# Optimization experiments

Measured on AMD Instinct MI355X. Metric: run time of the kernel, lower is better.

The kernel has to match this reference:

```python
import jax, jax.numpy as jnp
import numpy as np


def setup_inputs() -> dict:
    key = jax.random.key(0)
    k1, k2, k3, k4, k5 = jax.random.split(key, 5)
    B, S, D, H, E = 4, 4096, 1024, 1024, 8  # H = per-expert hidden (fuel_dim)
    std = 0.02
    return {
        "hidden_states": jax.random.normal(k1, (B, S, D), dtype=jnp.float32),
        "gate_w": jax.random.normal(k2, (D, E), dtype=jnp.float32) * std,
        "gw": jax.random.normal(k3, (E, D, H), dtype=jnp.float32) * std,
        "pw": jax.random.normal(k4, (E, D, H), dtype=jnp.float32) * std,
        "ow": jax.random.normal(k5, (E, H, D), dtype=jnp.float32) * std,
        "top_k": 2,
    }


def reference(hidden_states, gate_w, gw, pw, ow, top_k):
    B, S, D = hidden_states.shape
    E = gate_w.shape[1]
    x = hidden_states.reshape(-1, D)  # [T, D]
    T = x.shape[0]

    # Router
    router_logits = x @ gate_w  # [T, E]
    routing_probs = jax.nn.softmax(router_logits.astype(jnp.float32), axis=-1)
    top_w, top_i = jax.lax.top_k(routing_probs, top_k)  # [T, k]
    top_w = top_w / jnp.sum(top_w, axis=-1, keepdims=True)
    top_w = top_w.astype(x.dtype)

    # Dense combine weights: zero for unselected experts -> same math as
    # the torch gather/expert/scatter loop.
    combine = jnp.zeros((T, E), dtype=x.dtype).at[
        jnp.arange(T)[:, None], top_i
    ].set(top_w)  # [T, E]

    # SwiGLU experts, batched over the expert dim.
    g = jnp.einsum('td,edh->eth', x, gw)          # [E, T, H]
    p = jnp.einsum('td,edh->eth', x, pw)          # [E, T, H]
    h = g * jax.nn.silu(p)                        # [E, T, H]
    y = jnp.einsum('eth,ehd->etd', h, ow)         # [E, T, D]
    final = jnp.einsum('etd,te->td', y, combine)  # [T, D]
    final = final.reshape(B, S, D)

    # Load-balancing loss (recomputes softmax/topk as the torch fn does)
    expert_mask = jax.nn.one_hot(top_i, E, dtype=jnp.float32)  # [T, k, E]
    tokens_per_expert = jnp.mean(expert_mask, axis=0)          # [k, E]
    router_prob_per_expert = jnp.mean(routing_probs, axis=0)   # [E]
    bl_loss = jnp.sum(tokens_per_expert * router_prob_per_expert[None, :]) * E

    return final, router_logits, bl_loss
```

## Files before the change

### kernel.cpp

```cpp
#include <hip/hip_runtime.h>
#include <hip/hip_bf16.h>
#include <cstdint>

#define T_TOK 16384
#define DDIM  1024

typedef __attribute__((ext_vector_type(8))) short bf16x8;
typedef __attribute__((ext_vector_type(4))) float f32x4;

__device__ __forceinline__ unsigned short f2bf(float f) {
  unsigned u = __builtin_bit_cast(unsigned, f);
  return (unsigned short)((u + 0x7fffu + ((u >> 16) & 1u)) >> 16);
}
__device__ __forceinline__ unsigned pk2(float a, float b) {
  return (unsigned)f2bf(a) | ((unsigned)f2bf(b) << 16);
}
__device__ __forceinline__ void gload16(const void* g, void* l) {
  typedef __attribute__((address_space(1))) const unsigned int gu32;
  typedef __attribute__((address_space(3))) unsigned int lu32;
  __builtin_amdgcn_global_load_lds((gu32*)g, (lu32*)l, 16, 0, 0);
}

#define SBAR()                        \
  __builtin_amdgcn_sched_barrier(0);  \
  __builtin_amdgcn_s_barrier();       \
  __builtin_amdgcn_sched_barrier(0)
#define WAIT_VM8()                                        \
  asm volatile("s_waitcnt vmcnt(8)" ::: "memory");        \
  __builtin_amdgcn_sched_barrier(0)
#define WAIT_VM0()                                        \
  asm volatile("s_waitcnt vmcnt(0)" ::: "memory");        \
  __builtin_amdgcn_sched_barrier(0)
#define WAIT_LGKM0()                                      \
  asm volatile("s_waitcnt lgkmcnt(0)" ::: "memory");      \
  __builtin_amdgcn_sched_barrier(0)

__global__ __launch_bounds__(256) void convert_k(
    const float* __restrict__ gw, const float* __restrict__ pw,
    const float* __restrict__ ow, char* __restrict__ wg,
    char* __restrict__ wp, char* __restrict__ wo) {
  __shared__ float t[64][65];
  const int z = blockIdx.z;
  const int arr = z >> 3, e = z & 7;
  const float* src = (arr == 0 ? gw : arr == 1 ? pw : ow) + ((long)e << 20);
  char* dst = (arr == 0 ? wg : arr == 1 ? wp : wo) + ((long)e << 21);
  const int r0 = blockIdx.x * 64, c0 = blockIdx.y * 64;
  const int row = threadIdx.x >> 2, q = threadIdx.x & 3;
  const float4* sp = (const float4*)(src + (long)(r0 + row) * 1024 + c0 + q * 16);
  float4 v0 = sp[0], v1 = sp[1], v2 = sp[2], v3 = sp[3];
  float* tr = &t[row][q * 16];
  tr[0]=v0.x; tr[1]=v0.y; tr[2]=v0.z; tr[3]=v0.w;
  tr[4]=v1.x; tr[5]=v1.y; tr[6]=v1.z; tr[7]=v1.w;
  tr[8]=v2.x; tr[9]=v2.y; tr[10]=v2.z; tr[11]=v2.w;
  tr[12]=v3.x; tr[13]=v3.y; tr[14]=v3.z; tr[15]=v3.w;
  __syncthreads();
  const int cl = row, rq = q;
  uint4 o0, o1;
  o0.x = pk2(t[rq*16+ 0][cl], t[rq*16+ 1][cl]);
  o0.y = pk2(t[rq*16+ 2][cl], t[rq*16+ 3][cl]);
  o0.z = pk2(t[rq*16+ 4][cl], t[rq*16+ 5][cl]);
  o0.w = pk2(t[rq*16+ 6][cl], t[rq*16+ 7][cl]);
  o1.x = pk2(t[rq*16+ 8][cl], t[rq*16+ 9][cl]);
  o1.y = pk2(t[rq*16+10][cl], t[rq*16+11][cl]);
  o1.z = pk2(t[rq*16+12][cl], t[rq*16+13][cl]);
  o1.w = pk2(t[rq*16+14][cl], t[rq*16+15][cl]);
  char* dp = dst + (long)(c0 + cl) * 2048 + (long)(r0 + rq * 16) * 2;
  *(uint4*)dp = o0;
  *(uint4*)(dp + 16) = o1;
}

__global__ __launch_bounds__(256) void router_k(
    const float* __restrict__ x, const float* __restrict__ gatew,
    float* __restrict__ logitsOut, float4* __restrict__ route,
    float* __restrict__ accum, unsigned short* __restrict__ xbo) {
  __shared__ float accB[16];
  const int tid = threadIdx.x;
  if (tid < 16) accB[tid] = 0.f;
  __syncthreads();
  const int lane = tid & 63;
  const int gwave = blockIdx.x * 4 + (tid >> 6);

  for (int g = gwave; g < 4096; g += 1024) {
    const int t0 = g * 4;
    float s[4][8];
#pragma unroll
    for (int tt = 0; tt < 4; ++tt)
#pragma unroll
      for (int e = 0; e < 8; ++e) s[tt][e] = 0.f;

    for (int i = 0; i < 16; ++i) {
      int d = lane + i * 64;
      float4 w0 = *(const float4*)(gatew + d * 8);
      float4 w1 = *(const float4*)(gatew + d * 8 + 4);
#pragma unroll
      for (int tt = 0; tt < 4; ++tt) {
        float xv = x[(long)(t0 + tt) * DDIM + d];
        if (xbo) xbo[(long)(t0 + tt) * DDIM + d] = f2bf(xv);
        s[tt][0] += xv * w0.x; s[tt][1] += xv * w0.y;
        s[tt][2] += xv * w0.z; s[tt][3] += xv * w0.w;
        s[tt][4] += xv * w1.x; s[tt][5] += xv * w1.y;
        s[tt][6] += xv * w1.z; s[tt][7] += xv * w1.w;
      }
    }
#pragma unroll
    for (int m = 1; m < 64; m <<= 1)
#pragma unroll
      for (int tt = 0; tt < 4; ++tt)
#pragma unroll
        for (int e = 0; e < 8; ++e) s[tt][e] += __shfl_xor(s[tt][e], m);

    float psum[8];
#pragma unroll
    for (int e = 0; e < 8; ++e) psum[e] = 0.f;
    int i1a[4], i2a[4];
    float w1a[4], w2a[4];
#pragma unroll
    for (int tt = 0; tt < 4; ++tt) {
      float mx = s[tt][0];
#pragma unroll
      for (int e = 1; e < 8; ++e) mx = fmaxf(mx, s[tt][e]);
      float pe[8], Z = 0.f;
#pragma unroll
      for (int e = 0; e < 8; ++e) { pe[e] = __expf(s[tt][e] - mx); Z += pe[e]; }
      float inv = 1.f / Z;
#pragma unroll
      for (int e = 0; e < 8; ++e) { pe[e] *= inv; psum[e] += pe[e]; }
      int i1 = 0; float p1 = pe[0];
#pragma unroll
      for (int e = 1; e < 8; ++e) if (pe[e] > p1) { p1 = pe[e]; i1 = e; }
      int i2 = -1; float p2 = -1.f;
#pragma unroll
      for (int e = 0; e < 8; ++e)
        if (e != i1 && pe[e] > p2) { p2 = pe[e]; i2 = e; }
      float wsum = p1 + p2;
      i1a[tt] = i1; i2a[tt] = i2;
      w1a[tt] = p1 / wsum; w2a[tt] = p2 / wsum;
    }
    if (lane < 32) {
      int tt = lane >> 3, e = lane & 7;
      logitsOut[(t0 + tt) * 8 + e] = s[tt][e];
    }
    if (lane < 32 && (lane & 7) == 0) {
      int tt = lane >> 3;
      float4 rr;
      rr.x = w1a[tt]; rr.y = w2a[tt];
      rr.z = __int_as_float(i1a[tt]); rr.w = __int_as_float(i2a[tt]);
      route[t0 + tt] = rr;
    }
    if (lane < 8) {
      float c = 0.f;
#pragma unroll
      for (int tt = 0; tt < 4; ++tt)
        c += (float)(i1a[tt] == lane) + (float)(i2a[tt] == lane);
      atomicAdd(&accB[lane], psum[lane]);
      atomicAdd(&accB[8 + lane], c);
    }
  }
  __syncthreads();
  if (tid < 16) atomicAdd(&accum[tid], accB[tid]);
}

__global__ void offsets_k(const float* __restrict__ accum,
                          int* __restrict__ offs, int* __restrict__ cursor,
                          int* __restrict__ cumT) {
  if (threadIdx.x == 0) {
    int c = 0;
#pragma unroll
    for (int e = 0; e < 8; ++e) {
      offs[e] = c; cursor[e] = c;
      c += (int)(accum[8 + e] + 0.5f);
    }
    offs[8] = c;
    int t = 0;
#pragma unroll
    for (int e = 0; e < 8; ++e) {
      cumT[e] = t;
      t += (offs[e + 1] - offs[e] + 255) >> 8;
    }
    cumT[8] = t;
  }
}

__global__ __launch_bounds__(256) void scatter_k(
    const float4* __restrict__ route, int* __restrict__ cursor,
    int* __restrict__ list, float* __restrict__ wsl) {
  int t = blockIdx.x * 256 + threadIdx.x;
  float4 rr = route[t];
  int i1 = __float_as_int(rr.z), i2 = __float_as_int(rr.w);
  int s1 = atomicAdd(&cursor[i1], 1);
  list[s1] = t; wsl[s1] = rr.x;
  int s2 = atomicAdd(&cursor[i2], 1);
  list[s2] = t; wsl[s2] = rr.y;
}

template <int XB>
__global__ __launch_bounds__(512, 2) void pass1_k(
    const float* __restrict__ x, const unsigned short* __restrict__ xb,
    const char* __restrict__ wg, const char* __restrict__ wp,
    const int* __restrict__ list, const float* __restrict__ wsl,
    const int* __restrict__ offs, const int* __restrict__ cumT,
    char* __restrict__ hw) {
  __shared__ __align__(16) char Al[2][32768];
  __shared__ __align__(16) char Bgl[2][16384];
  __shared__ __align__(16) char Bpl[2][16384];
  const int b = blockIdx.x;
  if (b >= cumT[8]) return;
  int e = 0;
#pragma unroll
  for (int i = 1; i < 8; ++i) e += (b >= cumT[i]);
  const int tile = b - cumT[e];
  const int start = offs[e] + tile * 256;
  const int valid = min(256, offs[e + 1] - start);
  const int chunk = blockIdx.y;
  const int tid = threadIdx.x, lane = tid & 63, wid = tid >> 6;

  const int l8 = lane >> 3, seg = lane & 7;
  const unsigned inrow = ((unsigned)(seg * 16)) ^ (((unsigned)l8) << 4);

  const char* asrc[4];
  unsigned adst[4];
#pragma unroll
  for (int i = 0; i < 4; ++i) {
    int row = wid * 32 + i * 8 + l8;
    int tok = list[start + min(row, valid - 1)];
    asrc[i] = (const char*)xb + ((long)tok << 11) + inrow;
    adst[i] = (unsigned)(wid * 4096 + i * 1024);
  }
  const long wbase = ((long)e << 21) + ((long)(chunk * 128) << 11);
  const char* gsrc[2];
  const char* psrc[2];
  unsigned bdst[2];
#pragma unroll
  for (int i = 0; i < 2; ++i) {
    int h = wid * 16 + i * 8 + l8;
    gsrc[i] = wg + wbase + ((long)h << 11) + inrow;
    psrc[i] = wp + wbase + ((long)h << 11) + inrow;
    bdst[i] = (unsigned)(wid * 2048 + i * 1024);
  }

  f32x4 aG[8][2], aP[8][2];
#pragma unroll
  for (int f = 0; f < 8; ++f)
#pragma unroll
    for (int j = 0; j < 2; ++j) {
      aG[f][j] = (f32x4){0.f, 0.f, 0.f, 0.f};
      aP[f][j] = (f32x4){0.f, 0.f, 0.f, 0.f};
    }

  const int col = lane & 15, kg = lane >> 4;
  const int mb = (wid >> 2) * 128, nb = (wid & 3) * 32;

#define P1_STAGE(kb, buf)                                     \
  {                                                           \
    long ko = (long)(kb) << 7;                                \
    gload16(asrc[0] + ko, &Al[buf][adst[0]]);                 \
    gload16(asrc[1] + ko, &Al[buf][adst[1]]);                 \
    gload16(asrc[2] + ko, &Al[buf][adst[2]]);                 \
    gload16(asrc[3] + ko, &Al[buf][adst[3]]);                 \
    gload16(gsrc[0] + ko, &Bgl[buf][bdst[0]]);                \
    gload16(gsrc[1] + ko, &Bgl[buf][bdst[1]]);                \
    gload16(psrc[0] + ko, &Bpl[buf][bdst[0]]);                \
    gload16(psrc[1] + ko, &Bpl[buf][bdst[1]]);                \
  }

  if (XB) {
    P1_STAGE(0, 0);
#pragma unroll 1
    for (int kb = 0; kb < 16; ++kb) {
      const int cur = kb & 1;
      if (kb < 15) {
        P1_STAGE(kb + 1, cur ^ 1);
        WAIT_VM8();
      } else {
        WAIT_VM0();
      }
      SBAR();
#pragma unroll
      for (int ks = 0; ks < 2; ++ks) {
        bf16x8 bg[2], bp[2], af[4];
#pragma unroll
        for (int j = 0; j < 2; ++j) {
          int n = nb + j * 16 + col;
          unsigned off = (unsigned)(n * 128 + ks * 64 + kg * 16) ^
                         (((unsigned)n & 7u) << 4);
          bg[j] = *(const bf16x8*)(&Bgl[cur][0] + off);
          bp[j] = *(const bf16x8*)(&Bpl[cur][0] + off);
        }
#pragma unroll
        for (int f = 0; f < 4; ++f) {
          int r = mb + f * 16 + col;
          af[f] = *(const bf16x8*)(
              &Al[cur][0] + ((unsigned)(r * 128 + ks * 64 + kg * 16) ^
                             (((unsigned)r & 7u) << 4)));
        }
        WAIT_LGKM0();
        __builtin_amdgcn_s_setprio(1);
#pragma unroll
        for (int f = 0; f < 4; ++f)
#pragma unroll
          for (int j = 0; j < 2; ++j) {
            aG[f][j] = __builtin_amdgcn_mfma_f32_16x16x32_bf16(
                af[f], bg[j], aG[f][j], 0, 0, 0);
            aP[f][j] = __builtin_amdgcn_mfma_f32_16x16x32_bf16(
                af[f], bp[j], aP[f][j], 0, 0, 0);
          }
        __builtin_amdgcn_s_setprio(0);
        SBAR();
#pragma unroll
        for (int f = 0; f < 4; ++f) {
          int r = mb + (f + 4) * 16 + col;
          af[f] = *(const bf16x8*)(
              &Al[cur][0] + ((unsigned)(r * 128 + ks * 64 + kg * 16) ^
                             (((unsigned)r & 7u) << 4)));
        }
        WAIT_LGKM0();
        __builtin_amdgcn_s_setprio(1);
#pragma unroll
        for (int f = 0; f < 4; ++f)
#pragma unroll
          for (int j = 0; j < 2; ++j) {
            aG[f + 4][j] = __builtin_amdgcn_mfma_f32_16x16x32_bf16(
                af[f], bg[j], aG[f + 4][j], 0, 0, 0);
            aP[f + 4][j] = __builtin_amdgcn_mfma_f32_16x16x32_bf16(
                af[f], bp[j], aP[f + 4][j], 0, 0, 0);
          }
        __builtin_amdgcn_s_setprio(0);
        SBAR();
      }
    }
  } else {
    const int sr2 = tid >> 1, q2 = tid & 1;
    const int tokS = list[start + min(sr2, valid - 1)];
    const float* axp = x + (long)tokS * DDIM + q2 * 32;
    const unsigned swzS = ((unsigned)(sr2 & 7)) << 4;
    const unsigned sbS = (unsigned)(sr2 * 128 + q2 * 64);
#pragma unroll 1
    for (int kb = 0; kb < 16; ++kb) {
      __syncthreads();
      {
        const float4* ap = (const float4*)(axp + kb * 64);
#pragma unroll
        for (int m = 0; m < 4; ++m) {
          float4 v0 = ap[m * 2], v1 = ap[m * 2 + 1];
          uint4 w;
          w.x = pk2(v0.x, v0.y); w.y = pk2(v0.z, v0.w);
          w.z = pk2(v1.x, v1.y); w.w = pk2(v1.z, v1.w);
          *(uint4*)(&Al[0][0] + ((sbS + m * 16) ^ swzS)) = w;
        }
        long ko = (long)kb << 7;
        gload16(gsrc[0] + ko, &Bgl[0][bdst[0]]);
        gload16(gsrc[1] + ko, &Bgl[0][bdst[1]]);
        gload16(psrc[0] + ko, &Bpl[0][bdst[0]]);
        gload16(psrc[1] + ko, &Bpl[0][bdst[1]]);
      }
      __syncthreads();
#pragma unroll
      for (int ks = 0; ks < 2; ++ks) {
        bf16x8 bg[2], bp[2];
#pragma unroll
        for (int j = 0; j < 2; ++j) {
          int n = nb + j * 16 + col;
          unsigned off = (unsigned)(n * 128 + ks * 64 + kg * 16) ^
                         (((unsigned)n & 7u) << 4);
          bg[j] = *(const bf16x8*)(&Bgl[0][0] + off);
          bp[j] = *(const bf16x8*)(&Bpl[0][0] + off);
        }
#pragma unroll
        for (int f = 0; f < 8; ++f) {
          int r = mb + f * 16 + col;
          bf16x8 a = *(const bf16x8*)(
              &Al[0][0] + ((unsigned)(r * 128 + ks * 64 + kg * 16) ^
                           (((unsigned)r & 7u) << 4)));
#pragma unroll
          for (int j = 0; j < 2; ++j) {
            aG[f][j] = __builtin_amdgcn_mfma_f32_16x16x32_bf16(
                a, bg[j], aG[f][j], 0, 0, 0);
            aP[f][j] = __builtin_amdgcn_mfma_f32_16x16x32_bf16(
                a, bp[j], aP[f][j], 0, 0, 0);
          }
        }
      }
    }
  }

  const int rg = lane >> 4;
#pragma unroll
  for (int f = 0; f < 8; ++f) {
#pragma unroll
    for (int r = 0; r < 4; ++r) {
      int ml = mb + f * 16 + rg * 4 + r;
      if (ml < valid) {
        int slot = start + ml;
        float wv = wsl[slot];
#pragma unroll
        for (int j = 0; j < 2; ++j) {
          float g = aG[f][j][r], p = aP[f][j][r];
          float h = g * (p / (1.f + __expf(-p))) * wv;
          int hc = chunk * 128 + nb + j * 16 + col;
          *(unsigned short*)(hw + (((long)slot << 11) + (hc << 1))) = f2bf(h);
        }
      }
    }
  }
}

__global__ __launch_bounds__(512, 2) void pass2_k(
    const char* __restrict__ hw, const char* __restrict__ wo,
    const int* __restrict__ list, const int* __restrict__ offs,
    const int* __restrict__ cumT, float* __restrict__ out) {
  __shared__ __align__(16) char Al[2][32768];
  __shared__ __align__(16) char Bl[2][32768];
  const int b = blockIdx.x;
  if (b >= cumT[8]) return;
  int e = 0;
#pragma unroll
  for (int i = 1; i < 8; ++i) e += (b >= cumT[i]);
  const int tile = b - cumT[e];
  const int start = offs[e] + tile * 256;
  const int valid = min(256, offs[e + 1] - start);
  const int chunk = blockIdx.y;
  const int tid = threadIdx.x, lane = tid & 63, wid = tid >> 6;

  const int l8 = lane >> 3, seg = lane & 7;
  const unsigned inrow = ((unsigned)(seg * 16)) ^ (((unsigned)l8) << 4);

  const char* asrc[4];
  const char* bsrc[4];
  unsigned dst4[4];
#pragma unroll
  for (int i = 0; i < 4; ++i) {
    int row = wid * 32 + i * 8 + l8;
    asrc[i] = hw + ((long)(start + min(row, valid - 1)) << 11) + inrow;
    bsrc[i] = wo + ((long)e << 21) + ((long)(chunk * 256 + row) << 11) + inrow;
    dst4[i] = (unsigned)(wid * 4096 + i * 1024);
  }

  f32x4 acc[8][4];
#pragma unroll
  for (int f = 0; f < 8; ++f)
#pragma unroll
    for (int j = 0; j < 4; ++j) acc[f][j] = (f32x4){0.f, 0.f, 0.f, 0.f};

  const int col = lane & 15, kg = lane >> 4;
  const int mb = (wid >> 2) * 128, nb = (wid & 3) * 64;

#define P2_STAGE(kb, buf)                                     \
  {                                                           \
    long ko = (long)(kb) << 7;                                \
    gload16(asrc[0] + ko, &Al[buf][dst4[0]]);                 \
    gload16(asrc[1] + ko, &Al[buf][dst4[1]]);                 \
    gload16(asrc[2] + ko, &Al[buf][dst4[2]]);                 \
    gload16(asrc[3] + ko, &Al[buf][dst4[3]]);                 \
    gload16(bsrc[0] + ko, &Bl[buf][dst4[0]]);                 \
    gload16(bsrc[1] + ko, &Bl[buf][dst4[1]]);                 \
    gload16(bsrc[2] + ko, &Bl[buf][dst4[2]]);                 \
    gload16(bsrc[3] + ko, &Bl[buf][dst4[3]]);                 \
  }

  P2_STAGE(0, 0);
#pragma unroll 1
  for (int kb = 0; kb < 16; ++kb) {
    const int cur = kb & 1;
    if (kb < 15) {
      P2_STAGE(kb + 1, cur ^ 1);
      WAIT_VM8();
    } else {
      WAIT_VM0();
    }
    SBAR();
#pragma unroll
    for (int ks = 0; ks < 2; ++ks) {
      bf16x8 bf4[4], af[4];
#pragma unroll
      for (int j = 0; j < 4; ++j) {
        int n = nb + j * 16 + col;
        bf4[j] = *(const bf16x8*)(
            &Bl[cur][0] + ((unsigned)(n * 128 + ks * 64 + kg * 16) ^
                           (((unsigned)n & 7u) << 4)));
      }
#pragma unroll
      for (int f = 0; f < 4; ++f) {
        int r = mb + f * 16 + col;
        af[f] = *(const bf16x8*)(
            &Al[cur][0] + ((unsigned)(r * 128 + ks * 64 + kg * 16) ^
                           (((unsigned)r & 7u) << 4)));
      }
      WAIT_LGKM0();
      __builtin_amdgcn_s_setprio(1);
#pragma unroll
      for (int f = 0; f < 4; ++f)
#pragma unroll
        for (int j = 0; j < 4; ++j)
          acc[f][j] = __builtin_amdgcn_mfma_f32_16x16x32_bf16(
              af[f], bf4[j], acc[f][j], 0, 0, 0);
      __builtin_amdgcn_s_setprio(0);
      SBAR();
#pragma unroll
      for (int f = 0; f < 4; ++f) {
        int r = mb + (f + 4) * 16 + col;
        af[f] = *(const bf16x8*)(
            &Al[cur][0] + ((unsigned)(r * 128 + ks * 64 + kg * 16) ^
                           (((unsigned)r & 7u) << 4)));
      }
      WAIT_LGKM0();
      __builtin_amdgcn_s_setprio(1);
#pragma unroll
      for (int f = 0; f < 4; ++f)
#pragma unroll
        for (int j = 0; j < 4; ++j)
          acc[f + 4][j] = __builtin_amdgcn_mfma_f32_16x16x32_bf16(
              af[f], bf4[j], acc[f + 4][j], 0, 0, 0);
      __builtin_amdgcn_s_setprio(0);
      SBAR();
    }
  }

  const int rg = lane >> 4;
#pragma unroll
  for (int f = 0; f < 8; ++f) {
#pragma unroll
    for (int r = 0; r < 4; ++r) {
      int ml = mb + f * 16 + rg * 4 + r;
      if (ml < valid) {
        int token = list[start + ml];
#pragma unroll
        for (int j = 0; j < 4; ++j) {
          int c = chunk * 256 + nb + j * 16 + col;
          atomicAdd(&out[(long)token * DDIM + c], acc[f][j][r]);
        }
      }
    }
  }
}

__global__ void loss_k(const float* __restrict__ accum, float* __restrict__ out) {
  if (threadIdx.x == 0 && blockIdx.x == 0) {
    float L = 0.f;
#pragma unroll
    for (int e = 0; e < 8; ++e) L += accum[e] * accum[8 + e];
    out[0] = L * 8.f / ((float)T_TOK * (float)T_TOK);
  }
}

extern "C" void kernel_launch(void* const* d_in, const int* in_sizes, int n_in,
                              void* d_out, int out_size, void* d_ws,
                              size_t ws_size, hipStream_t stream) {
  const float* x     = (const float*)d_in[0];
  const float* gatew = (const float*)d_in[1];
  const float* gw    = (const float*)d_in[2];
  const float* pw    = (const float*)d_in[3];
  const float* ow    = (const float*)d_in[4];

  float* out       = (float*)d_out;
  float* logitsOut = out + (long)T_TOK * DDIM;
  float* lossOut   = out + (long)T_TOK * DDIM + T_TOK * 8;

  char* wsB = (char*)d_ws;
  float*  accum  = (float*)wsB;
  int*    cursor = (int*)(wsB + 64);
  int*    offs   = (int*)(wsB + 96);
  int*    cumT   = (int*)(wsB + 160);
  float4* route  = (float4*)(wsB + 1024);
  int*    list   = (int*)(wsB + 263168);
  float*  wsl    = (float*)(wsB + 394240);
  char*   wg     = wsB + (1l << 20);
  char*   wp     = wsB + 17825792;
  char*   wo     = wsB + 34603008;
  char*   hw     = wsB + 51380224;
  unsigned short* xb = (unsigned short*)(wsB + 118489088);
  const bool big = ws_size >= 152043520ul;

  hipMemsetAsync(d_out, 0, (size_t)out_size * 4, stream);
  hipMemsetAsync(accum, 0, 64, stream);
  convert_k<<<dim3(16, 16, 24), 256, 0, stream>>>(gw, pw, ow, wg, wp, wo);
  router_k<<<256, 256, 0, stream>>>(x, gatew, logitsOut, route, accum,
                                    big ? xb : nullptr);
  offsets_k<<<1, 64, 0, stream>>>(accum, offs, cursor, cumT);
  scatter_k<<<64, 256, 0, stream>>>(route, cursor, list, wsl);
  if (big)
    pass1_k<1><<<dim3(136, 8), 512, 0, stream>>>(x, xb, wg, wp, list, wsl,
                                                 offs, cumT, hw);
  else
    pass1_k<0><<<dim3(136, 8), 512, 0, stream>>>(x, xb, wg, wp, list, wsl,
                                                 offs, cumT, hw);
  pass2_k<<<dim3(136, 4), 512, 0, stream>>>(hw, wo, list, offs, cumT, out);
  loss_k<<<1, 64, 0, stream>>>(accum, lossOut);
}
```

Baseline: 732.6 us.

## Split staged loads across compute phases and replace output atomics with combine kernel

In both grouped GEMM passes, each k-block's global-to-LDS loads are split into four parts issued between MFMA phases, waiting only on the first part, so loads overlap compute more finely. When workspace is large enough, pass2 writes per-slot bf16 results to a buffer instead of atomically adding to the fp32 output. A new combine kernel then sums each token's two expert rows using slot indices recorded by scatter, which also removes the output memset. This avoids atomic contention at the cost of an extra bf16 round trip and an additional kernel. Rounding partial outputs to bf16 adds some precision loss.

```diff
diff --git a/kernel.cpp b/kernel.cpp
--- a/kernel.cpp
+++ b/kernel.cpp
@@ -14,6 +14,12 @@
 }
 __device__ __forceinline__ unsigned pk2(float a, float b) {
   return (unsigned)f2bf(a) | ((unsigned)f2bf(b) << 16);
+}
+__device__ __forceinline__ float bflo(unsigned u) {
+  return __uint_as_float(u << 16);
+}
+__device__ __forceinline__ float bfhi(unsigned u) {
+  return __uint_as_float(u & 0xffff0000u);
 }
 __device__ __forceinline__ void gload16(const void* g, void* l) {
   typedef __attribute__((address_space(1))) const unsigned int gu32;
@@ -25,8 +31,8 @@
   __builtin_amdgcn_sched_barrier(0);  \
   __builtin_amdgcn_s_barrier();       \
   __builtin_amdgcn_sched_barrier(0)
-#define WAIT_VM8()                                        \
-  asm volatile("s_waitcnt vmcnt(8)" ::: "memory");        \
+#define WAIT_VM2()                                        \
+  asm volatile("s_waitcnt vmcnt(2)" ::: "memory");        \
   __builtin_amdgcn_sched_barrier(0)
 #define WAIT_VM0()                                        \
   asm volatile("s_waitcnt vmcnt(0)" ::: "memory");        \
@@ -183,7 +189,8 @@
 
 __global__ __launch_bounds__(256) void scatter_k(
     const float4* __restrict__ route, int* __restrict__ cursor,
-    int* __restrict__ list, float* __restrict__ wsl) {
+    int* __restrict__ list, float* __restrict__ wsl,
+    int* __restrict__ slots) {
   int t = blockIdx.x * 256 + threadIdx.x;
   float4 rr = route[t];
   int i1 = __float_as_int(rr.z), i2 = __float_as_int(rr.w);
@@ -191,6 +198,7 @@
   list[s1] = t; wsl[s1] = rr.x;
   int s2 = atomicAdd(&cursor[i2], 1);
   list[s2] = t; wsl[s2] = rr.y;
+  slots[t * 2] = s1; slots[t * 2 + 1] = s2;
 }
 
 template <int XB>
@@ -250,27 +258,33 @@
   const int col = lane & 15, kg = lane >> 4;
   const int mb = (wid >> 2) * 128, nb = (wid & 3) * 32;
 
-#define P1_STAGE(kb, buf)                                     \
+#define P1_PART(kb, buf, part)                                \
   {                                                           \
     long ko = (long)(kb) << 7;                                \
-    gload16(asrc[0] + ko, &Al[buf][adst[0]]);                 \
-    gload16(asrc[1] + ko, &Al[buf][adst[1]]);                 \
-    gload16(asrc[2] + ko, &Al[buf][adst[2]]);                 \
-    gload16(asrc[3] + ko, &Al[buf][adst[3]]);                 \
-    gload16(gsrc[0] + ko, &Bgl[buf][bdst[0]]);                \
-    gload16(gsrc[1] + ko, &Bgl[buf][bdst[1]]);                \
-    gload16(psrc[0] + ko, &Bpl[buf][bdst[0]]);                \
-    gload16(psrc[1] + ko, &Bpl[buf][bdst[1]]);                \
+    if ((part) == 0) {                                        \
+      gload16(asrc[0] + ko, &Al[buf][adst[0]]);               \
+      gload16(asrc[1] + ko, &Al[buf][adst[1]]);               \
+    } else if ((part) == 1) {                                 \
+      gload16(asrc[2] + ko, &Al[buf][adst[2]]);               \
+      gload16(asrc[3] + ko, &Al[buf][adst[3]]);               \
+    } else if ((part) == 2) {                                 \
+      gload16(gsrc[0] + ko, &Bgl[buf][bdst[0]]);              \
+      gload16(gsrc[1] + ko, &Bgl[buf][bdst[1]]);              \
+    } else {                                                  \
+      gload16(psrc[0] + ko, &Bpl[buf][bdst[0]]);              \
+      gload16(psrc[1] + ko, &Bpl[buf][bdst[1]]);              \
+    }                                                         \
   }
 
   if (XB) {
-    P1_STAGE(0, 0);
+    P1_PART(0, 0, 0); P1_PART(0, 0, 1); P1_PART(0, 0, 2); P1_PART(0, 0, 3);
 #pragma unroll 1
     for (int kb = 0; kb < 16; ++kb) {
-      const int cur = kb & 1;
+      const int cur = kb & 1, nxt = cur ^ 1;
+      SBAR();
       if (kb < 15) {
-        P1_STAGE(kb + 1, cur ^ 1);
-        WAIT_VM8();
+        P1_PART(kb + 1, nxt, 0);
+        WAIT_VM2();
       } else {
         WAIT_VM0();
       }
@@ -293,6 +307,8 @@
               &Al[cur][0] + ((unsigned)(r * 128 + ks * 64 + kg * 16) ^
                              (((unsigned)r & 7u) << 4)));
         }
+        if (kb < 15 && (2 * ks) < 3) P1_PART(kb + 1, nxt, 2 * ks + 1);
+        SBAR();
         WAIT_LGKM0();
         __builtin_amdgcn_s_setprio(1);
 #pragma unroll
@@ -305,7 +321,6 @@
                 af[f], bp[j], aP[f][j], 0, 0, 0);
           }
         __builtin_amdgcn_s_setprio(0);
-        SBAR();
 #pragma unroll
         for (int f = 0; f < 4; ++f) {
           int r = mb + (f + 4) * 16 + col;
@@ -313,6 +328,8 @@
               &Al[cur][0] + ((unsigned)(r * 128 + ks * 64 + kg * 16) ^
                              (((unsigned)r & 7u) << 4)));
         }
+        if (kb < 15 && (2 * ks + 1) < 3) P1_PART(kb + 1, nxt, 2 * ks + 2);
+        SBAR();
         WAIT_LGKM0();
         __builtin_amdgcn_s_setprio(1);
 #pragma unroll
@@ -325,7 +342,6 @@
                 af[f], bp[j], aP[f + 4][j], 0, 0, 0);
           }
         __builtin_amdgcn_s_setprio(0);
-        SBAR();
       }
     }
   } else {
@@ -404,10 +420,12 @@
   }
 }
 
+template <int ATOMIC>
 __global__ __launch_bounds__(512, 2) void pass2_k(
     const char* __restrict__ hw, const char* __restrict__ wo,
     const int* __restrict__ list, const int* __restrict__ offs,
-    const int* __restrict__ cumT, float* __restrict__ out) {
+    const int* __restrict__ cumT, float* __restrict__ out,
+    unsigned short* __restrict__ hw2) {
   __shared__ __align__(16) char Al[2][32768];
   __shared__ __align__(16) char Bl[2][32768];
   const int b = blockIdx.x;
@@ -444,26 +462,32 @@
   const int col = lane & 15, kg = lane >> 4;
   const int mb = (wid >> 2) * 128, nb = (wid & 3) * 64;
 
-#define P2_STAGE(kb, buf)                                     \
+#define P2_PART(kb, buf, part)                                \
   {                                                           \
     long ko = (long)(kb) << 7;                                \
-    gload16(asrc[0] + ko, &Al[buf][dst4[0]]);                 \
-    gload16(asrc[1] + ko, &Al[buf][dst4[1]]);                 \
-    gload16(asrc[2] + ko, &Al[buf][dst4[2]]);                 \
-    gload16(asrc[3] + ko, &Al[buf][dst4[3]]);                 \
-    gload16(bsrc[0] + ko, &Bl[buf][dst4[0]]);                 \
-    gload16(bsrc[1] + ko, &Bl[buf][dst4[1]]);                 \
-    gload16(bsrc[2] + ko, &Bl[buf][dst4[2]]);                 \
-    gload16(bsrc[3] + ko, &Bl[buf][dst4[3]]);                 \
-  }
-
-  P2_STAGE(0, 0);
+    if ((part) == 0) {                                        \
+      gload16(asrc[0] + ko, &Al[buf][dst4[0]]);               \
+      gload16(asrc[1] + ko, &Al[buf][dst4[1]]);               \
+    } else if ((part) == 1) {                                 \
+      gload16(asrc[2] + ko, &Al[buf][dst4[2]]);               \
+      gload16(asrc[3] + ko, &Al[buf][dst4[3]]);               \
+    } else if ((part) == 2) {                                 \
+      gload16(bsrc[0] + ko, &Bl[buf][dst4[0]]);               \
+      gload16(bsrc[1] + ko, &Bl[buf][dst4[1]]);               \
+    } else {                                                  \
+      gload16(bsrc[2] + ko, &Bl[buf][dst4[2]]);               \
+      gload16(bsrc[3] + ko, &Bl[buf][dst4[3]]);               \
+    }                                                         \
+  }
+
+  P2_PART(0, 0, 0); P2_PART(0, 0, 1); P2_PART(0, 0, 2); P2_PART(0, 0, 3);
 #pragma unroll 1
   for (int kb = 0; kb < 16; ++kb) {
-    const int cur = kb & 1;
+    const int cur = kb & 1, nxt = cur ^ 1;
+    SBAR();
     if (kb < 15) {
-      P2_STAGE(kb + 1, cur ^ 1);
-      WAIT_VM8();
+      P2_PART(kb + 1, nxt, 0);
+      WAIT_VM2();
     } else {
       WAIT_VM0();
     }
@@ -485,6 +509,8 @@
             &Al[cur][0] + ((unsigned)(r * 128 + ks * 64 + kg * 16) ^
                            (((unsigned)r & 7u) << 4)));
       }
+      if (kb < 15 && (2 * ks) < 3) P2_PART(kb + 1, nxt, 2 * ks + 1);
+      SBAR();
       WAIT_LGKM0();
       __builtin_amdgcn_s_setprio(1);
 #pragma unroll
@@ -494,7 +520,6 @@
           acc[f][j] = __builtin_amdgcn_mfma_f32_16x16x32_bf16(
               af[f], bf4[j], acc[f][j], 0, 0, 0);
       __builtin_amdgcn_s_setprio(0);
-      SBAR();
 #pragma unroll
       for (int f = 0; f < 4; ++f) {
         int r = mb + (f + 4) * 16 + col;
@@ -502,6 +527,8 @@
             &Al[cur][0] + ((unsigned)(r * 128 + ks * 64 + kg * 16) ^
                            (((unsigned)r & 7u) << 4)));
       }
+      if (kb < 15 && (2 * ks + 1) < 3) P2_PART(kb + 1, nxt, 2 * ks + 2);
+      SBAR();
       WAIT_LGKM0();
       __builtin_amdgcn_s_setprio(1);
 #pragma unroll
@@ -511,7 +538,6 @@
           acc[f + 4][j] = __builtin_amdgcn_mfma_f32_16x16x32_bf16(
               af[f], bf4[j], acc[f + 4][j], 0, 0, 0);
       __builtin_amdgcn_s_setprio(0);
-      SBAR();
     }
   }
 
@@ -522,15 +548,37 @@
     for (int r = 0; r < 4; ++r) {
       int ml = mb + f * 16 + rg * 4 + r;
       if (ml < valid) {
-        int token = list[start + ml];
+        int slot = start + ml;
 #pragma unroll
         for (int j = 0; j < 4; ++j) {
           int c = chunk * 256 + nb + j * 16 + col;
-          atomicAdd(&out[(long)token * DDIM + c], acc[f][j][r]);
-        }
-      }
-    }
-  }
+          if (ATOMIC) {
+            atomicAdd(&out[(long)list[slot] * DDIM + c], acc[f][j][r]);
+          } else {
+            hw2[((long)slot << 10) + c] = f2bf(acc[f][j][r]);
+          }
+        }
+      }
+    }
+  }
+}
+
+__global__ __launch_bounds__(128) void combine_k(
+    const unsigned short* __restrict__ hw2, const int* __restrict__ slots,
+    float* __restrict__ out) {
+  const int t = blockIdx.x;
+  const int s1 = slots[t * 2], s2 = slots[t * 2 + 1];
+  const int c = threadIdx.x;
+  uint4 a = *(const uint4*)(hw2 + ((long)s1 << 10) + c * 8);
+  uint4 b = *(const uint4*)(hw2 + ((long)s2 << 10) + c * 8);
+  float4 o0, o1;
+  o0.x = bflo(a.x) + bflo(b.x); o0.y = bfhi(a.x) + bfhi(b.x);
+  o0.z = bflo(a.y) + bflo(b.y); o0.w = bfhi(a.y) + bfhi(b.y);
+  o1.x = bflo(a.z) + bflo(b.z); o1.y = bfhi(a.z) + bfhi(b.z);
+  o1.z = bflo(a.w) + bflo(b.w); o1.w = bfhi(a.w) + bfhi(b.w);
+  float* op = out + (long)t * DDIM + c * 8;
+  *(float4*)op = o0;
+  *(float4*)(op + 4) = o1;
 }
 
 __global__ void loss_k(const float* __restrict__ accum, float* __restrict__ out) {
@@ -563,26 +611,36 @@
   float4* route  = (float4*)(wsB + 1024);
   int*    list   = (int*)(wsB + 263168);
   float*  wsl    = (float*)(wsB + 394240);
+  int*    slots  = (int*)(wsB + 525312);
   char*   wg     = wsB + (1l << 20);
   char*   wp     = wsB + 17825792;
   char*   wo     = wsB + 34603008;
   char*   hw     = wsB + 51380224;
-  unsigned short* xb = (unsigned short*)(wsB + 118489088);
-  const bool big = ws_size >= 152043520ul;
-
-  hipMemsetAsync(d_out, 0, (size_t)out_size * 4, stream);
+  unsigned short* xb  = (unsigned short*)(wsB + 118489088);
+  unsigned short* hw2 = (unsigned short*)(wsB + 152043520);
+  const bool big  = ws_size >= 152043520ul;
+  const bool comb = ws_size >= 219152384ul;
+
+  if (!comb) hipMemsetAsync(d_out, 0, (size_t)out_size * 4, stream);
   hipMemsetAsync(accum, 0, 64, stream);
   convert_k<<<dim3(16, 16, 24), 256, 0, stream>>>(gw, pw, ow, wg, wp, wo);
   router_k<<<256, 256, 0, stream>>>(x, gatew, logitsOut, route, accum,
                                     big ? xb : nullptr);
   offsets_k<<<1, 64, 0, stream>>>(accum, offs, cursor, cumT);
-  scatter_k<<<64, 256, 0, stream>>>(route, cursor, list, wsl);
+  scatter_k<<<64, 256, 0, stream>>>(route, cursor, list, wsl, slots);
   if (big)
     pass1_k<1><<<dim3(136, 8), 512, 0, stream>>>(x, xb, wg, wp, list, wsl,
                                                  offs, cumT, hw);
   else
     pass1_k<0><<<dim3(136, 8), 512, 0, stream>>>(x, xb, wg, wp, list, wsl,
                                                  offs, cumT, hw);
-  pass2_k<<<dim3(136, 4), 512, 0, stream>>>(hw, wo, list, offs, cumT, out);
+  if (comb) {
+    pass2_k<0><<<dim3(136, 4), 512, 0, stream>>>(hw, wo, list, offs, cumT,
+                                                 out, hw2);
+    combine_k<<<T_TOK, 128, 0, stream>>>(hw2, slots, out);
+  } else {
+    pass2_k<1><<<dim3(136, 4), 512, 0, stream>>>(hw, wo, list, offs, cumT,
+                                                 out, hw2);
+  }
   loss_k<<<1, 64, 0, stream>>>(accum, lossOut);
 }
```

New measurement: 621.1 us. -15.2%, faster.
